# Kernel optimization log

Hardware: AMD Instinct MI355X
Metric: run time of the kernel (lower is better)

## Reference

```python
import jax, jax.numpy as jnp
import numpy as np

N_ITER = 50  # bisection iterations (matches entmax_bisect default)


def entmax_bisect(x, alpha):
    """alpha-entmax via bisection along axis=1. x: [B, L, 1], alpha: [1] (>1)."""
    a_m1 = alpha - 1.0
    inv = 1.0 / a_m1
    xs = x * a_m1
    d = x.shape[1]
    max_val = jnp.max(xs, axis=1, keepdims=True)
    tau_lo = max_val - 1.0
    tau_hi = max_val - (1.0 / d) ** a_m1
    f_lo = jnp.sum(jnp.maximum(xs - tau_lo, 0.0) ** inv, axis=1, keepdims=True) - 1.0

    def body(i, carry):
        tau_lo, dm = carry
        dm = dm * 0.5
        tau_m = tau_lo + dm
        f_m = jnp.sum(jnp.maximum(xs - tau_m, 0.0) ** inv, axis=1, keepdims=True) - 1.0
        tau_lo = jnp.where(f_m * f_lo >= 0.0, tau_m, tau_lo)
        return (tau_lo, dm)

    tau_lo, dm = jax.lax.fori_loop(0, N_ITER, body, (tau_lo, tau_hi - tau_lo))
    p = jnp.maximum(xs - (tau_lo + 0.5 * dm), 0.0) ** inv
    return p / jnp.sum(p, axis=1, keepdims=True)


def setup_inputs() -> dict:
    key = jax.random.key(0)
    ks = jax.random.split(key, 8)
    B, L, E2, D = 256, 512, 512, 256  # E2 = emb_size * 2
    C_target = jax.random.normal(ks[0], (B, E2), jnp.float32)
    C = jax.random.normal(ks[1], (B, L, E2), jnp.float32)
    X = jax.random.normal(ks[2], (B, E2, D), jnp.float32)
    alpha = jnp.array([1.5], jnp.float32)  # entmax-1.5
    mask = jax.random.randint(ks[3], (B, L), 0, 2, jnp.int32).at[:, 0].set(1)
    s = 1.0 / np.sqrt(E2)
    Wg1 = jax.random.uniform(ks[4], (E2, E2), jnp.float32, -s, s)
    Wg2 = jax.random.uniform(ks[5], (E2, E2), jnp.float32, -s, s)
    Wg0 = jax.random.uniform(ks[6], (E2, 1), jnp.float32, -s, s)
    bias_alpha = jax.random.normal(ks[7], (E2,), jnp.float32) * 0.02
    return dict(C_target=C_target, C=C, X=X, alpha=alpha, mask=mask,
                Wg1=Wg1, Wg2=Wg2, Wg0=Wg0, bias_alpha=bias_alpha)


def reference(C_target, C, X, alpha, mask, Wg1, Wg2, Wg0, bias_alpha):
    q = C_target[:, None, :]                               # [B, 1, 2E]
    h = jax.nn.relu(C @ Wg1 + q @ Wg2 + bias_alpha)        # [B, L, 2E]
    score = h @ Wg0                                        # [B, L, 1]
    score = jnp.where(mask[..., None] == 0, -1e30, score)  # mask -> -inf
    p = entmax_bisect(score, alpha)                        # sparse attn over L
    attn = jnp.swapaxes(p, 1, 2) @ C                       # [B, 1, 2E]
    out = jnp.sum(attn @ X, axis=1)                        # [B, D]
    return out
```

## Files before the change

kernel.cpp:

```cpp
#include <hip/hip_runtime.h>
#include <hip/hip_bf16.h>

typedef __bf16 bf16_t;
typedef bf16_t bf16x8 __attribute__((ext_vector_type(8)));
typedef float f32x4 __attribute__((ext_vector_type(4)));

#define AS1 __attribute__((address_space(1)))
#define AS3 __attribute__((address_space(3)))

__global__ __launch_bounds__(256) void k_prep(const float* __restrict__ Wg1,
                                              bf16_t* __restrict__ W3,
                                              const float* __restrict__ Ct,
                                              const float* __restrict__ Wg2,
                                              const float* __restrict__ bias,
                                              float* __restrict__ g,
                                              const int* __restrict__ mask,
                                              int* __restrict__ idx,
                                              int* __restrict__ nnz) {
    const int bid = blockIdx.x;
    const int t   = threadIdx.x;
    if (bid < 128) {
        const int slot = bid * 256 + t;
        const int K3   = slot >> 9;
        const int n    = slot & 511;
        union { bf16_t h[8]; uint4 u; } pk;
        #pragma unroll
        for (int j = 0; j < 8; ++j)
            pk.h[j] = (bf16_t)Wg1[(K3 * 8 + j) * 512 + n];
        *reinterpret_cast<uint4*>(W3 + (size_t)slot * 8) = pk.u;
    } else if (bid < 640) {
        __shared__ float q[512];
        const int gb = bid - 128;
        const int b  = gb >> 1;
        q[t]       = Ct[b * 512 + t];
        q[t + 256] = Ct[b * 512 + t + 256];
        __syncthreads();
        const int e = ((gb & 1) << 8) + t;
        float acc = bias[e];
        #pragma unroll 16
        for (int k = 0; k < 512; ++k)
            acc = fmaf(q[k], Wg2[k * 512 + e], acc);
        g[b * 512 + e] = acc;
    } else {
        const int b = bid - 640;
        if (t < 64) {
            const int lane = t;
            int base = 0;
            #pragma unroll
            for (int c = 0; c < 8; ++c) {
                const int l = (c << 6) + lane;
                const int v = mask[(b << 9) + l];
                const unsigned long long m = __ballot(v != 0);
                const int rank = __popcll(m & ((1ull << lane) - 1ull));
                if (v) idx[(b << 9) + base + rank] = l;
                base += __popcll(m);
            }
            if (lane == 0) nnz[b] = base;
        }
    }
}

__global__ __launch_bounds__(256, 3) void k_score(const float* __restrict__ C,
                                                  const bf16_t* __restrict__ W3,
                                                  const float* __restrict__ g,
                                                  const float* __restrict__ Wg0,
                                                  const int* __restrict__ idx,
                                                  const int* __restrict__ nnz,
                                                  float* __restrict__ scoreh) {
    __shared__ __align__(16) bf16_t Bs[2][4 * 256 * 8];
    __shared__ __align__(16) bf16_t As[2][4 * 64 * 8];
    __shared__ float sred[4][64];

    const int t    = threadIdx.x;
    const int lane = t & 63;
    const int wave = t >> 6;
    const int quad = lane >> 4;
    const int l15  = lane & 15;

    const int bid  = blockIdx.x;
    const int nh   = bid & 1;
    const int tl   = bid >> 1;
    const int b    = tl >> 3;
    const int tile = tl & 7;
    const int nb   = nnz[b];
    if (tile * 64 >= nb) return;

    const int ncol0 = nh << 8;

    const int arow = t & 63;
    const int aq   = t >> 6;
    const int ja   = tile * 64 + arow;
    const int ra   = idx[(b << 9) + (ja < nb ? ja : nb - 1)];
    const float* Ca = C + ((size_t)b << 18) + (size_t)ra * 512 + aq * 8;

    float4 a0 = *reinterpret_cast<const float4*>(Ca);
    float4 a1 = *reinterpret_cast<const float4*>(Ca + 4);
    {
        union { bf16_t h[8]; uint4 u; } pk;
        pk.h[0] = (bf16_t)a0.x; pk.h[1] = (bf16_t)a0.y;
        pk.h[2] = (bf16_t)a0.z; pk.h[3] = (bf16_t)a0.w;
        pk.h[4] = (bf16_t)a1.x; pk.h[5] = (bf16_t)a1.y;
        pk.h[6] = (bf16_t)a1.z; pk.h[7] = (bf16_t)a1.w;
        *reinterpret_cast<uint4*>(&As[0][(aq * 64 + arow) * 8]) = pk.u;
    }
    a0 = *reinterpret_cast<const float4*>(Ca + 32);
    a1 = *reinterpret_cast<const float4*>(Ca + 36);
    #pragma unroll
    for (int i = 0; i < 4; ++i)
        __builtin_amdgcn_global_load_lds(
            (const AS1 void*)(W3 + ((size_t)(i * 512) + ncol0 + t) * 8),
            (AS3 void*)(&Bs[0][(i * 256 + t) * 8]), 16, 0, 0);
    __syncthreads();

    f32x4 acc[4][4] = {};

    #pragma unroll
    for (int kc = 0; kc < 16; ++kc) {
        const int c = kc & 1;
        if (kc < 15) {
            #pragma unroll
            for (int i = 0; i < 4; ++i)
                __builtin_amdgcn_global_load_lds(
                    (const AS1 void*)(W3 + ((size_t)((kc + 1) * 4 + i) * 512
                                            + ncol0 + t) * 8),
                    (AS3 void*)(&Bs[c ^ 1][(i * 256 + t) * 8]), 16, 0, 0);
            union { bf16_t h[8]; uint4 u; } pk;
            pk.h[0] = (bf16_t)a0.x; pk.h[1] = (bf16_t)a0.y;
            pk.h[2] = (bf16_t)a0.z; pk.h[3] = (bf16_t)a0.w;
            pk.h[4] = (bf16_t)a1.x; pk.h[5] = (bf16_t)a1.y;
            pk.h[6] = (bf16_t)a1.z; pk.h[7] = (bf16_t)a1.w;
            *reinterpret_cast<uint4*>(&As[c ^ 1][(aq * 64 + arow) * 8]) = pk.u;
        }
        if (kc < 14) {
            a0 = *reinterpret_cast<const float4*>(Ca + (kc + 2) * 32);
            a1 = *reinterpret_cast<const float4*>(Ca + (kc + 2) * 32 + 4);
        }
        bf16x8 afr[4], bfr[4];
        #pragma unroll
        for (int mi = 0; mi < 4; ++mi)
            afr[mi] = *reinterpret_cast<const bf16x8*>(
                &As[c][(quad * 64 + mi * 16 + l15) * 8]);
        #pragma unroll
        for (int ni = 0; ni < 4; ++ni)
            bfr[ni] = *reinterpret_cast<const bf16x8*>(
                &Bs[c][(quad * 256 + wave * 64 + ni * 16 + l15) * 8]);
        #pragma unroll
        for (int mi = 0; mi < 4; ++mi)
            #pragma unroll
            for (int ni = 0; ni < 4; ++ni)
                acc[mi][ni] = __builtin_amdgcn_mfma_f32_16x16x32_bf16(
                    afr[mi], bfr[ni], acc[mi][ni], 0, 0, 0);
        __syncthreads();
    }

    float rsum[16];
    #pragma unroll
    for (int i = 0; i < 16; ++i) rsum[i] = 0.f;
    #pragma unroll
    for (int ni = 0; ni < 4; ++ni) {
        const int n  = ncol0 + wave * 64 + ni * 16 + l15;
        const float gv = g[(b << 9) + n];
        const float w0 = Wg0[n];
        #pragma unroll
        for (int mi = 0; mi < 4; ++mi)
            #pragma unroll
            for (int r = 0; r < 4; ++r) {
                const float u = fmaxf(acc[mi][ni][r] + gv, 0.f);
                rsum[mi * 4 + r] = fmaf(u, w0, rsum[mi * 4 + r]);
            }
    }
    #pragma unroll
    for (int i = 0; i < 16; ++i) {
        float v = rsum[i];
        v += __shfl_xor(v, 1);
        v += __shfl_xor(v, 2);
        v += __shfl_xor(v, 4);
        v += __shfl_xor(v, 8);
        rsum[i] = v;
    }
    if (l15 == 0) {
        #pragma unroll
        for (int mi = 0; mi < 4; ++mi)
            #pragma unroll
            for (int r = 0; r < 4; ++r)
                sred[wave][mi * 16 + quad * 4 + r] = rsum[mi * 4 + r];
    }
    __syncthreads();
    if (t < 64) {
        const int j = tile * 64 + t;
        if (j < nb) {
            const float sc = sred[0][t] + sred[1][t] + sred[2][t] + sred[3][t];
            scoreh[((size_t)nh << 17) + (b << 9) + idx[(b << 9) + j]] = sc;
        }
    }
}

__global__ __launch_bounds__(256) void k_post(const float* __restrict__ scoreh,
                                              const int* __restrict__ mask,
                                              const float* __restrict__ alpha,
                                              const float* __restrict__ C,
                                              const float* __restrict__ X,
                                              float* __restrict__ out) {
    __shared__ float sup_v[512];
    __shared__ int   sup_i[512];
    __shared__ int   s_n;
    __shared__ float attn_s[512];
    __shared__ f32x4 red[4][64];

    const int b = blockIdx.x;
    const int t = threadIdx.x;

    if (t < 64) {
        const int lane = t;
        const float am1 = alpha[0] - 1.0f;
        const float inv = 1.0f / am1;
        const bool  sq  = fabsf(inv - 2.0f) < 1e-6f;
        const float neg = -1e30f * am1;

        const float* s0 = scoreh + (b << 9);
        const float* s1 = scoreh + (1u << 17) + (b << 9);
        const int*   mb = mask   + (b << 9);
        float x[8];
        {
            const float4 u0 = *reinterpret_cast<const float4*>(s0 + lane * 8);
            const float4 u1 = *reinterpret_cast<const float4*>(s0 + lane * 8 + 4);
            const float4 w0 = *reinterpret_cast<const float4*>(s1 + lane * 8);
            const float4 w1 = *reinterpret_cast<const float4*>(s1 + lane * 8 + 4);
            const int4   m0 = *reinterpret_cast<const int4*>(mb + lane * 8);
            const int4   m1 = *reinterpret_cast<const int4*>(mb + lane * 8 + 4);
            x[0] = m0.x ? (u0.x + w0.x) * am1 : neg;
            x[1] = m0.y ? (u0.y + w0.y) * am1 : neg;
            x[2] = m0.z ? (u0.z + w0.z) * am1 : neg;
            x[3] = m0.w ? (u0.w + w0.w) * am1 : neg;
            x[4] = m1.x ? (u1.x + w1.x) * am1 : neg;
            x[5] = m1.y ? (u1.y + w1.y) * am1 : neg;
            x[6] = m1.z ? (u1.z + w1.z) * am1 : neg;
            x[7] = m1.w ? (u1.w + w1.w) * am1 : neg;
        }
        float m = x[0];
        #pragma unroll
        for (int j = 1; j < 8; ++j) m = fmaxf(m, x[j]);
        #pragma unroll
        for (int s = 1; s < 64; s <<= 1) m = fmaxf(m, __shfl_xor(m, s));

        float tau_lo = m - 1.0f;
        float dm = (m - powf(1.0f / 512.0f, am1)) - tau_lo;

        float f_lo;
        {
            float s = 0.f;
            #pragma unroll
            for (int j = 0; j < 8; ++j) {
                const float u = fmaxf(x[j] - tau_lo, 0.f);
                s += sq ? u * u : powf(u, inv);
            }
            #pragma unroll
            for (int sh = 1; sh < 64; sh <<= 1) s += __shfl_xor(s, sh);
            f_lo = s - 1.0f;
        }
        for (int it = 0; it < 50; ++it) {
            dm *= 0.5f;
            const float tau_m = tau_lo + dm;
            float s = 0.f;
            #pragma unroll
            for (int j = 0; j < 8; ++j) {
                const float u = fmaxf(x[j] - tau_m, 0.f);
                s += sq ? u * u : powf(u, inv);
            }
            #pragma unroll
            for (int sh = 1; sh < 64; sh <<= 1) s += __shfl_xor(s, sh);
            if ((s - 1.0f) * f_lo >= 0.f) tau_lo = tau_m;
        }
        const float tau = tau_lo + 0.5f * dm;
        float pj[8];
        float Z = 0.f;
        #pragma unroll
        for (int j = 0; j < 8; ++j) {
            const float u = fmaxf(x[j] - tau, 0.f);
            pj[j] = sq ? u * u : powf(u, inv);
            Z += pj[j];
        }
        #pragma unroll
        for (int sh = 1; sh < 64; sh <<= 1) Z += __shfl_xor(Z, sh);
        const float rz = 1.0f / Z;

        int base = 0;
        #pragma unroll
        for (int j = 0; j < 8; ++j) {
            const float pv = pj[j] * rz;
            const unsigned long long bm = __ballot(pv > 0.f);
            const int rank = __popcll(bm & ((1ull << lane) - 1ull));
            if (pv > 0.f) {
                sup_i[base + rank] = lane * 8 + j;
                sup_v[base + rank] = pv;
            }
            base += __popcll(bm);
        }
        if (lane == 0) s_n = base;
    }
    __syncthreads();

    const int n = s_n;
    const float* Cb = C + ((size_t)b << 18);
    float a0 = 0.f, a1 = 0.f;
    int j = 0;
    for (; j + 4 <= n; j += 4) {
        #pragma unroll
        for (int u = 0; u < 4; ++u) {
            const float  w  = sup_v[j + u];
            const float* cr = Cb + ((size_t)sup_i[j + u] << 9);
            a0 = fmaf(w, cr[t], a0);
            a1 = fmaf(w, cr[t + 256], a1);
        }
    }
    for (; j < n; ++j) {
        const float  w  = sup_v[j];
        const float* cr = Cb + ((size_t)sup_i[j] << 9);
        a0 = fmaf(w, cr[t], a0);
        a1 = fmaf(w, cr[t + 256], a1);
    }
    attn_s[t]       = a0;
    attn_s[t + 256] = a1;
    __syncthreads();

    const int eg = t >> 6;
    const int d4 = t & 63;
    const float4* Xb = reinterpret_cast<const float4*>(X + ((size_t)b << 17));
    f32x4 a = {};
    #pragma unroll 8
    for (int e = eg; e < 512; e += 4) {
        const float  w = attn_s[e];
        const float4 v = Xb[e * 64 + d4];
        a[0] = fmaf(w, v.x, a[0]);
        a[1] = fmaf(w, v.y, a[1]);
        a[2] = fmaf(w, v.z, a[2]);
        a[3] = fmaf(w, v.w, a[3]);
    }
    red[eg][d4] = a;
    __syncthreads();
    if (t < 64) {
        const f32x4 s = red[0][t] + red[1][t] + red[2][t] + red[3][t];
        float4 o;
        o.x = s[0]; o.y = s[1]; o.z = s[2]; o.w = s[3];
        *reinterpret_cast<float4*>(out + (b << 8) + (t << 2)) = o;
    }
}

extern "C" void kernel_launch(void* const* d_in, const int* in_sizes, int n_in,
                              void* d_out, int out_size, void* d_ws, size_t ws_size,
                              hipStream_t stream) {
    const float* C_target = (const float*)d_in[0];
    const float* C        = (const float*)d_in[1];
    const float* X        = (const float*)d_in[2];
    const float* alpha    = (const float*)d_in[3];
    const int*   mask     = (const int*)  d_in[4];
    const float* Wg1      = (const float*)d_in[5];
    const float* Wg2      = (const float*)d_in[6];
    const float* Wg0      = (const float*)d_in[7];
    const float* bias     = (const float*)d_in[8];
    float* out = (float*)d_out;

    char* ws = (char*)d_ws;
    bf16_t* w3     = (bf16_t*)(ws);
    float*  g      = (float*)(ws + ( 512u << 10));
    float*  scoreh = (float*)(ws + (1024u << 10));
    int*    idx    = (int*)  (ws + (2048u << 10));
    int*    nnz    = (int*)  (ws + (2560u << 10));

    k_prep  <<<896, 256, 0, stream>>>(Wg1, w3, C_target, Wg2, bias, g,
                                      mask, idx, nnz);
    k_score <<<4096, 256, 0, stream>>>(C, w3, g, Wg0, idx, nnz, scoreh);
    k_post  <<<256, 256, 0, stream>>>(scoreh, mask, alpha, C, X, out);
}
```

Before: 592.6 us.

## Give each wave its own 16 rows and feed A operand from registers

Reorganizes k_score so each wave owns 16 gathered C rows across all 256 columns, loading its A fragment straight from global into registers and converting to bf16 in-register. This drops the shared-memory A staging buffer and the cross-wave score reduction through shared memory. Synchronization switches to explicit waitcnt plus s_barrier with sched_barriers for finer pipelining control. In exchange, every wave now reads the full B tile from LDS (more LDS read traffic per MFMA), and the hand-counted vmcnt values must stay correct.

New measurement: 565.6 us. -4.6%, faster.

```diff
diff --git a/kernel.cpp b/kernel.cpp
--- a/kernel.cpp
+++ b/kernel.cpp
@@ -68,8 +68,6 @@
                                                   const int* __restrict__ nnz,
                                                   float* __restrict__ scoreh) {
     __shared__ __align__(16) bf16_t Bs[2][4 * 256 * 8];
-    __shared__ __align__(16) bf16_t As[2][4 * 64 * 8];
-    __shared__ float sred[4][64];
 
     const int t    = threadIdx.x;
     const int lane = t & 63;
@@ -87,36 +85,40 @@
 
     const int ncol0 = nh << 8;
 
-    const int arow = t & 63;
-    const int aq   = t >> 6;
-    const int ja   = tile * 64 + arow;
-    const int ra   = idx[(b << 9) + (ja < nb ? ja : nb - 1)];
-    const float* Ca = C + ((size_t)b << 18) + (size_t)ra * 512 + aq * 8;
-
-    float4 a0 = *reinterpret_cast<const float4*>(Ca);
-    float4 a1 = *reinterpret_cast<const float4*>(Ca + 4);
-    {
-        union { bf16_t h[8]; uint4 u; } pk;
-        pk.h[0] = (bf16_t)a0.x; pk.h[1] = (bf16_t)a0.y;
-        pk.h[2] = (bf16_t)a0.z; pk.h[3] = (bf16_t)a0.w;
-        pk.h[4] = (bf16_t)a1.x; pk.h[5] = (bf16_t)a1.y;
-        pk.h[6] = (bf16_t)a1.z; pk.h[7] = (bf16_t)a1.w;
-        *reinterpret_cast<uint4*>(&As[0][(aq * 64 + arow) * 8]) = pk.u;
-    }
-    a0 = *reinterpret_cast<const float4*>(Ca + 32);
-    a1 = *reinterpret_cast<const float4*>(Ca + 36);
+    const int ja = tile * 64 + wave * 16 + l15;
+    const int ra = idx[(b << 9) + (ja < nb ? ja : nb - 1)];
+    const float* Ca = C + ((size_t)b << 18) + (size_t)ra * 512 + (quad << 3);
+
     #pragma unroll
     for (int i = 0; i < 4; ++i)
         __builtin_amdgcn_global_load_lds(
-            (const AS1 void*)(W3 + ((size_t)(i * 512) + ncol0 + t) * 8),
+            (const AS1 void*)(W3 + ((size_t)i * 512 + ncol0 + t) * 8),
             (AS3 void*)(&Bs[0][(i * 256 + t) * 8]), 16, 0, 0);
-    __syncthreads();
-
-    f32x4 acc[4][4] = {};
+    __builtin_amdgcn_sched_barrier(0);
+    float4 va[2][2];
+    va[0][0] = *reinterpret_cast<const float4*>(Ca);
+    va[0][1] = *reinterpret_cast<const float4*>(Ca + 4);
+    va[1][0] = *reinterpret_cast<const float4*>(Ca + 32);
+    va[1][1] = *reinterpret_cast<const float4*>(Ca + 36);
+    __builtin_amdgcn_sched_barrier(0);
+    asm volatile("s_waitcnt vmcnt(4)" ::: "memory");
+    __builtin_amdgcn_s_barrier();
+    __builtin_amdgcn_sched_barrier(0);
+
+    f32x4 acc[16] = {};
 
     #pragma unroll
     for (int kc = 0; kc < 16; ++kc) {
         const int c = kc & 1;
+        union { bf16_t h[8]; bf16x8 v; } ua;
+        {
+            const float4 A0 = va[c][0], A1 = va[c][1];
+            ua.h[0] = (bf16_t)A0.x; ua.h[1] = (bf16_t)A0.y;
+            ua.h[2] = (bf16_t)A0.z; ua.h[3] = (bf16_t)A0.w;
+            ua.h[4] = (bf16_t)A1.x; ua.h[5] = (bf16_t)A1.y;
+            ua.h[6] = (bf16_t)A1.z; ua.h[7] = (bf16_t)A1.w;
+        }
+        __builtin_amdgcn_sched_barrier(0);
         if (kc < 15) {
             #pragma unroll
             for (int i = 0; i < 4; ++i)
@@ -124,73 +126,68 @@
                     (const AS1 void*)(W3 + ((size_t)((kc + 1) * 4 + i) * 512
                                             + ncol0 + t) * 8),
                     (AS3 void*)(&Bs[c ^ 1][(i * 256 + t) * 8]), 16, 0, 0);
-            union { bf16_t h[8]; uint4 u; } pk;
-            pk.h[0] = (bf16_t)a0.x; pk.h[1] = (bf16_t)a0.y;
-            pk.h[2] = (bf16_t)a0.z; pk.h[3] = (bf16_t)a0.w;
-            pk.h[4] = (bf16_t)a1.x; pk.h[5] = (bf16_t)a1.y;
-            pk.h[6] = (bf16_t)a1.z; pk.h[7] = (bf16_t)a1.w;
-            *reinterpret_cast<uint4*>(&As[c ^ 1][(aq * 64 + arow) * 8]) = pk.u;
-        }
+        }
+        __builtin_amdgcn_sched_barrier(0);
         if (kc < 14) {
-            a0 = *reinterpret_cast<const float4*>(Ca + (kc + 2) * 32);
-            a1 = *reinterpret_cast<const float4*>(Ca + (kc + 2) * 32 + 4);
-        }
-        bf16x8 afr[4], bfr[4];
-        #pragma unroll
-        for (int mi = 0; mi < 4; ++mi)
-            afr[mi] = *reinterpret_cast<const bf16x8*>(
-                &As[c][(quad * 64 + mi * 16 + l15) * 8]);
-        #pragma unroll
-        for (int ni = 0; ni < 4; ++ni)
-            bfr[ni] = *reinterpret_cast<const bf16x8*>(
-                &Bs[c][(quad * 256 + wave * 64 + ni * 16 + l15) * 8]);
-        #pragma unroll
-        for (int mi = 0; mi < 4; ++mi)
-            #pragma unroll
-            for (int ni = 0; ni < 4; ++ni)
-                acc[mi][ni] = __builtin_amdgcn_mfma_f32_16x16x32_bf16(
-                    afr[mi], bfr[ni], acc[mi][ni], 0, 0, 0);
-        __syncthreads();
-    }
-
-    float rsum[16];
+            va[c][0] = *reinterpret_cast<const float4*>(Ca + (kc + 2) * 32);
+            va[c][1] = *reinterpret_cast<const float4*>(Ca + (kc + 2) * 32 + 4);
+        }
+        __builtin_amdgcn_sched_barrier(0);
+        #pragma unroll
+        for (int g2 = 0; g2 < 2; ++g2) {
+            bf16x8 bfr[8];
+            #pragma unroll
+            for (int ni = 0; ni < 8; ++ni)
+                bfr[ni] = *reinterpret_cast<const bf16x8*>(
+                    &Bs[c][(quad * 256 + (g2 * 8 + ni) * 16 + l15) * 8]);
+            #pragma unroll
+            for (int ni = 0; ni < 8; ++ni)
+                acc[g2 * 8 + ni] = __builtin_amdgcn_mfma_f32_16x16x32_bf16(
+                    ua.v, bfr[ni], acc[g2 * 8 + ni], 0, 0, 0);
+        }
+        if (kc < 14) {
+            __builtin_amdgcn_sched_barrier(0);
+            asm volatile("s_waitcnt lgkmcnt(0)" ::: "memory");
+            asm volatile("s_waitcnt vmcnt(2)" ::: "memory");
+            __builtin_amdgcn_s_barrier();
+            __builtin_amdgcn_sched_barrier(0);
+        } else if (kc == 14) {
+            __builtin_amdgcn_sched_barrier(0);
+            asm volatile("s_waitcnt lgkmcnt(0)" ::: "memory");
+            asm volatile("s_waitcnt vmcnt(0)" ::: "memory");
+            __builtin_amdgcn_s_barrier();
+            __builtin_amdgcn_sched_barrier(0);
+        }
+    }
+
+    float rsum[4] = {0.f, 0.f, 0.f, 0.f};
     #pragma unroll
-    for (int i = 0; i < 16; ++i) rsum[i] = 0.f;
-    #pragma unroll
-    for (int ni = 0; ni < 4; ++ni) {
-        const int n  = ncol0 + wave * 64 + ni * 16 + l15;
+    for (int ni = 0; ni < 16; ++ni) {
+        const int n  = ncol0 + (ni << 4) + l15;
         const float gv = g[(b << 9) + n];
         const float w0 = Wg0[n];
         #pragma unroll
-        for (int mi = 0; mi < 4; ++mi)
-            #pragma unroll
-            for (int r = 0; r < 4; ++r) {
-                const float u = fmaxf(acc[mi][ni][r] + gv, 0.f);
-                rsum[mi * 4 + r] = fmaf(u, w0, rsum[mi * 4 + r]);
-            }
+        for (int r = 0; r < 4; ++r) {
+            const float u = fmaxf(acc[ni][r] + gv, 0.f);
+            rsum[r] = fmaf(u, w0, rsum[r]);
+        }
     }
     #pragma unroll
-    for (int i = 0; i < 16; ++i) {
-        float v = rsum[i];
+    for (int r = 0; r < 4; ++r) {
+        float v = rsum[r];
         v += __shfl_xor(v, 1);
         v += __shfl_xor(v, 2);
         v += __shfl_xor(v, 4);
         v += __shfl_xor(v, 8);
-        rsum[i] = v;
+        rsum[r] = v;
     }
     if (l15 == 0) {
         #pragma unroll
-        for (int mi = 0; mi < 4; ++mi)
-            #pragma unroll
-            for (int r = 0; r < 4; ++r)
-                sred[wave][mi * 16 + quad * 4 + r] = rsum[mi * 4 + r];
-    }
-    __syncthreads();
-    if (t < 64) {
-        const int j = tile * 64 + t;
-        if (j < nb) {
-            const float sc = sred[0][t] + sred[1][t] + sred[2][t] + sred[3][t];
-            scoreh[((size_t)nh << 17) + (b << 9) + idx[(b << 9) + j]] = sc;
+        for (int r = 0; r < 4; ++r) {
+            const int j = tile * 64 + wave * 16 + quad * 4 + r;
+            if (j < nb)
+                scoreh[((size_t)nh << 17) + (b << 9) + idx[(b << 9) + j]]
+                    = rsum[r];
         }
     }
 }
```
